# Kernel tuning notes

Measured on AMD Instinct MI355X. Metric: run time of the kernel, lower is better.

The kernel has to match this reference:

```python
import jax, jax.numpy as jnp
from jax import lax
import numpy as np

N_CLASS = 5
B, T = 2048, 2048


def setup_inputs() -> dict:
    key = jax.random.key(0)
    k1, k2 = jax.random.split(key)
    x = jax.random.normal(k1, (B, T, N_CLASS), dtype=jnp.float32)
    mask = jnp.ones((B, T), dtype=jnp.int32)
    transform = jax.random.normal(k2, (N_CLASS + 2, N_CLASS + 2), dtype=jnp.float32)
    return {"x": x, "mask": mask, "transform": transform}


def reference(x, mask, transform):
    # Batched Viterbi decode. x:[B,T,C], mask:[B,T], transform:[C+2,C+2]
    Bb, Tt, C = x.shape
    START, END = C, C + 1
    trans = transform[:C, :C]                      # [C,C] prev -> curr
    mb = mask.astype(bool)

    dp0 = x[:, 0, :] + transform[START, :C][None]  # [B,C]

    def step(dp, inp):
        xt, mt = inp                               # xt:[B,C], mt:[B]
        sc = dp[:, :, None] + trans[None]          # [B,C_prev,C_curr]
        bp = jnp.argmax(sc, axis=1)                # [B,C]
        new_dp = jnp.max(sc, axis=1) + xt          # [B,C]
        dp_out = jnp.where(mt[:, None], new_dp, dp)
        # identity backpointer on padded steps so backtrace is a no-op there
        bp_out = jnp.where(mt[:, None], bp, jnp.arange(C)[None, :])
        return dp_out, bp_out

    xs = (jnp.moveaxis(x[:, 1:, :], 1, 0),         # [T-1,B,C]
          jnp.moveaxis(mb[:, 1:], 1, 0))           # [T-1,B]
    dp, bps = lax.scan(step, dp0, xs)              # bps: [T-1,B,C]

    final = dp + transform[:C, END][None]          # [B,C]
    max_score = jnp.max(final, axis=1)             # [B]
    last = jnp.argmax(final, axis=1)               # [B]

    def back(idx, bp):
        prev = jnp.take_along_axis(bp, idx[:, None], axis=1)[:, 0]
        return prev, idx

    first, rest = lax.scan(back, last, bps, reverse=True)  # rest: [T-1,B]
    path = jnp.concatenate([first[None], rest], axis=0)    # [T,B]
    return max_score, path.T                                # [B], [B,T]
```

## Files before the change

### kernel.cpp

```cpp
#include <hip/hip_runtime.h>
#include <cstdint>

#define B_    2048
#define T_    2048
#define TD    7
#define NCHK  128
#define IDENT 0x4688u

__device__ __forceinline__ uint32_t mcompose(uint32_t f, uint32_t g) {
    uint32_t r = 0;
#pragma unroll
    for (int j = 0; j < 5; ++j) {
        uint32_t gj = (g >> (3 * j)) & 7u;
        r |= ((f >> (3 * gj)) & 7u) << (3 * j);
    }
    return r;
}

__device__ __forceinline__ uint32_t cvtpk(float lo, float hi) {
    uint32_t r;
    asm("v_cvt_pk_bf16_f32 %0, %1, %2" : "=v"(r) : "v"(lo), "v"(hi));
    return r;
}

__device__ __forceinline__ float bfld(const uint16_t* __restrict__ xs, int h) {
    return __uint_as_float(((uint32_t)xs[h]) << 16);
}

template<bool P>
__device__ __forceinline__ void hstep(const uint16_t* __restrict__ xs, int h, bool pred,
                                      float (&dp)[5], const float (&tr)[5][5]) {
    float nd[5];
#pragma unroll
    for (int j = 0; j < 5; ++j) {
        float v = fmaxf(fmaxf(fmaxf(fmaxf(dp[0] + tr[0][j], dp[1] + tr[1][j]),
                                    dp[2] + tr[2][j]), dp[3] + tr[3][j]),
                        dp[4] + tr[4][j]);
        nd[j] = v + bfld(xs, h + j);
    }
#pragma unroll
    for (int j = 0; j < 5; ++j) dp[j] = (P && !pred) ? dp[j] : nd[j];
}

template<bool SEL>
__device__ __forceinline__ uint32_t lstep(const uint16_t* __restrict__ xs, int h, bool mm,
                                          float (&dp)[5], const float (&tr)[5][5],
                                          uint32_t& rho) {
    float nd[5]; int aa[5]; uint32_t pk = 0;
#pragma unroll
    for (int j = 0; j < 5; ++j) {
        float s[5];
#pragma unroll
        for (int i = 0; i < 5; ++i) {
            float f = dp[i] + tr[i][j];
            uint32_t u = (__float_as_uint(f) & ~7u) | (uint32_t)(7 - i);
            s[i] = __uint_as_float(u);
        }
        float m = fmaxf(fmaxf(fmaxf(fmaxf(s[0], s[1]), s[2]), s[3]), s[4]);
        int a = 7 - (int)(__float_as_uint(m) & 7u);
        float v = m + bfld(xs, h + j);
        if (SEL) { a = mm ? a : j; nd[j] = mm ? v : dp[j]; }
        else     { nd[j] = v; }
        aa[j] = a;
        pk |= ((uint32_t)a) << (3 * j);
    }
    uint32_t nr = 0;
#pragma unroll
    for (int j = 0; j < 5; ++j) nr |= ((rho >> (3 * aa[j])) & 7u) << (3 * j);
    rho = nr;
#pragma unroll
    for (int j = 0; j < 5; ++j) dp[j] = nd[j];
    return pk;
}

template<bool AM>
__device__ __forceinline__ void fwd(const uint16_t* __restrict__ xs,
                                    const uint16_t* __restrict__ msk, int cc,
                                    const float (&tr)[5][5], const float (&ts)[5],
                                    float (&dp)[5], float (&dpE)[5],
                                    uint32_t (&acc)[8], uint32_t& rho) {
    const int hbase = (cc > 0) ? 82 * (cc - 1) : 0;
#pragma unroll
    for (int j = 0; j < 5; ++j) dp[j] = bfld(xs, hbase + j);
    if (cc <= 1) {
#pragma unroll
        for (int j = 0; j < 5; ++j) dp[j] += ts[j];
    }
    const uint32_t mh = AM ? 0xFFFFu : ((cc > 0) ? (uint32_t)msk[cc - 1] : 0u);
#pragma unroll
    for (int h = 1; h <= 15; ++h) {
        if (AM) hstep<false>(xs, hbase + 5 * h, true, dp, tr);
        else    hstep<true >(xs, hbase + 5 * h, ((mh >> h) & 1u) != 0, dp, tr);
    }
    if (AM && cc == 0) {
#pragma unroll
        for (int j = 0; j < 5; ++j) dp[j] = bfld(xs, j) + ts[j];
    }
#pragma unroll
    for (int j = 0; j < 5; ++j) dpE[j] = (cc == 0) ? 0.0f : dp[j];

    rho = IDENT;
    const int lb = 82 * cc;
    const uint32_t ml = AM ? 0xFFFFu : (uint32_t)msk[cc];
    acc[0] = lstep<true>(xs, lb, (cc != 0) && ((ml & 1u) != 0), dp, tr, rho);
#pragma unroll
    for (int l = 1; l < 16; ++l) {
        uint32_t pk;
        if (AM) pk = lstep<false>(xs, lb + 5 * l, true, dp, tr, rho);
        else    pk = lstep<true >(xs, lb + 5 * l, ((ml >> l) & 1u) != 0, dp, tr, rho);
        if (l & 1) acc[l >> 1] |= pk << 16;
        else       acc[l >> 1]  = pk;
    }
}

__global__ __launch_bounds__(128, 3) void k_all(
    const float* __restrict__ x, const int* __restrict__ mask,
    const float* __restrict__ tf, float* __restrict__ out)
{
    __shared__ uint16_t xs[10496];
    __shared__ uint16_t msk[NCHK];
    __shared__ uint32_t tot[2];
    __shared__ float    part[2];
    __shared__ int      lastS;

    const int b = blockIdx.x, c = threadIdx.x;
    const int lane = c & 63, w = c >> 6;

    const float4* gx = (const float4*)(x + (size_t)b * (T_ * 5));
    const int4*   gm = (const int4*)(mask + (size_t)b * T_);

    float4 va[10]; int4 m4[4];
#pragma unroll
    for (int q = 0; q < 10; ++q) va[q] = gx[c + 128 * q];
#pragma unroll
    for (int q = 0; q < 4; ++q) m4[q] = gm[4 * c + q];
    __builtin_amdgcn_sched_barrier(0);
    float4 vb[10];
#pragma unroll
    for (int q = 0; q < 10; ++q) vb[q] = gx[c + 128 * (10 + q)];
    __builtin_amdgcn_sched_barrier(0);

#pragma unroll
    for (int q = 0; q < 10; ++q) {
        int fi = c + 128 * q;
        int e0 = 4 * fi;
        int k  = (e0 * 52429) >> 22;
        int h0 = e0 + 2 * k;
        *(uint32_t*)(xs + h0)     = cvtpk(va[q].x, va[q].y);
        *(uint32_t*)(xs + h0 + 2) = cvtpk(va[q].z, va[q].w);
    }
    uint32_t mb = 0;
#pragma unroll
    for (int q = 0; q < 4; ++q) {
        mb |= (m4[q].x ? 1u : 0u) << (4 * q);
        mb |= (m4[q].y ? 1u : 0u) << (4 * q + 1);
        mb |= (m4[q].z ? 1u : 0u) << (4 * q + 2);
        mb |= (m4[q].w ? 1u : 0u) << (4 * q + 3);
    }
    msk[c] = (uint16_t)mb;
#pragma unroll
    for (int q = 0; q < 10; ++q) {
        int fi = c + 128 * (10 + q);
        int e0 = 4 * fi;
        int k  = (e0 * 52429) >> 22;
        int h0 = e0 + 2 * k;
        *(uint32_t*)(xs + h0)     = cvtpk(vb[q].x, vb[q].y);
        *(uint32_t*)(xs + h0 + 2) = cvtpk(vb[q].z, vb[q].w);
    }

    float tr[5][5], ts[5], te[5];
#pragma unroll
    for (int i = 0; i < 5; ++i)
#pragma unroll
        for (int j = 0; j < 5; ++j) tr[i][j] = tf[i * TD + j];
#pragma unroll
    for (int j = 0; j < 5; ++j) ts[j] = tf[5 * TD + j];
#pragma unroll
    for (int j = 0; j < 5; ++j) te[j] = tf[j * TD + 6];

    const int allones = __syncthreads_and(mb == 0xFFFFu);

    float dp[5], dpE[5]; uint32_t acc[8], rho;
    if (allones) fwd<true >(xs, msk, c, tr, ts, dp, dpE, acc, rho);
    else         fwd<false>(xs, msk, c, tr, ts, dp, dpE, acc, rho);

    float svec[5];
#pragma unroll
    for (int j = 0; j < 5; ++j) {
        int r = (rho >> (3 * j)) & 7;
        float e = dpE[0];
        e = (r == 1) ? dpE[1] : e;
        e = (r == 2) ? dpE[2] : e;
        e = (r == 3) ? dpE[3] : e;
        e = (r == 4) ? dpE[4] : e;
        svec[j] = dp[j] - e;
    }

    uint32_t I = rho;
#pragma unroll
    for (int d = 1; d < 64; d <<= 1) {
        uint32_t oth = __shfl_down(I, d);
        uint32_t cm  = mcompose(I, oth);
        I = (lane + d < 64) ? cm : I;
    }
    if (lane == 0) tot[w] = I;
    if (c == NCHK - 1) {
        float best = dp[0] + te[0]; int last = 0;
#pragma unroll
        for (int j = 1; j < 5; ++j) {
            float s = dp[j] + te[j];
            if (s > best) { best = s; last = j; }
        }
        lastS = last;
    }
    __syncthreads();

    uint32_t Tw = (w == 0) ? tot[1] : IDENT;
    uint32_t Ex = __shfl_down(I, 1);
    uint32_t M  = (lane < 63) ? mcompose(Ex, Tw) : Tw;
    const int last = lastS;
    const int ec = (M >> (3 * last)) & 7;

    {
        float v = svec[0];
        v = (ec == 1) ? svec[1] : v;
        v = (ec == 2) ? svec[2] : v;
        v = (ec == 3) ? svec[3] : v;
        v = (ec == 4) ? svec[4] : v;
        if (c == NCHK - 1) v += te[last];
#pragma unroll
        for (int off = 1; off < 64; off <<= 1) v += __shfl_xor(v, off);
        if (lane == 0) part[w] = v;
    }
    __syncthreads();
    if (c == 0) out[b] = part[0] + part[1];

    float pv[16];
    int e = ec;
#pragma unroll
    for (int l = 15; l >= 0; --l) {
        pv[l] = (float)e;
        uint32_t p = (acc[l >> 1] >> (16 * (l & 1))) & 0xFFFFu;
        e = (p >> (3 * e)) & 7;
    }
    float* path = out + B_ + (size_t)b * T_ + c * 16;
#pragma unroll
    for (int q = 0; q < 4; ++q) {
        float4 v; v.x = pv[4*q]; v.y = pv[4*q+1]; v.z = pv[4*q+2]; v.w = pv[4*q+3];
        ((float4*)path)[q] = v;
    }
}

extern "C" void kernel_launch(void* const* d_in, const int* in_sizes, int n_in,
                              void* d_out, int out_size, void* d_ws, size_t ws_size,
                              hipStream_t stream) {
    const float* x         = (const float*)d_in[0];
    const int*   mask      = (const int*)d_in[1];
    const float* transform = (const float*)d_in[2];
    float*       out       = (float*)d_out;

    hipLaunchKernelGGL(k_all, dim3(B_), dim3(128), 0, stream,
                       x, mask, transform, out);
}
```

Before: 38.71 us.

## Preload per-chunk bf16 inputs into registers via 16-byte LDS reads

Changes the shared-memory padding so each 80-element chunk starts on a 16-byte boundary (stride 88 halves). Each thread then loads its two chunks (halo and local) into 40-word register arrays with vectorized uint4 reads, replacing many scalar 16-bit LDS loads. Global-to-LDS stores become 8-byte writes, the sched barriers are dropped, and launch bounds drop from 3 to 2 waves per EU to make room for the extra 80 registers. The trade is fewer LDS instructions against higher register pressure and lower occupancy.

```diff
diff --git a/kernel.cpp b/kernel.cpp
--- a/kernel.cpp
+++ b/kernel.cpp
@@ -23,12 +23,14 @@
     return r;
 }
 
-__device__ __forceinline__ float bfld(const uint16_t* __restrict__ xs, int h) {
-    return __uint_as_float(((uint32_t)xs[h]) << 16);
-}
+__device__ __forceinline__ float xget(const uint32_t (&w)[40], int h) {
+    return (h & 1) ? __uint_as_float(w[h >> 1] & 0xFFFF0000u)
+                   : __uint_as_float(w[h >> 1] << 16);
+}
+
 
 template<bool P>
-__device__ __forceinline__ void hstep(const uint16_t* __restrict__ xs, int h, bool pred,
+__device__ __forceinline__ void hstep(const uint32_t (&w)[40], int base, bool pred,
                                       float (&dp)[5], const float (&tr)[5][5]) {
     float nd[5];
 #pragma unroll
@@ -36,14 +38,14 @@
         float v = fmaxf(fmaxf(fmaxf(fmaxf(dp[0] + tr[0][j], dp[1] + tr[1][j]),
                                     dp[2] + tr[2][j]), dp[3] + tr[3][j]),
                         dp[4] + tr[4][j]);
-        nd[j] = v + bfld(xs, h + j);
+        nd[j] = v + xget(w, base + j);
     }
 #pragma unroll
     for (int j = 0; j < 5; ++j) dp[j] = (P && !pred) ? dp[j] : nd[j];
 }
 
 template<bool SEL>
-__device__ __forceinline__ uint32_t lstep(const uint16_t* __restrict__ xs, int h, bool mm,
+__device__ __forceinline__ uint32_t lstep(const uint32_t (&w)[40], int base, bool mm,
                                           float (&dp)[5], const float (&tr)[5][5],
                                           uint32_t& rho) {
     float nd[5]; int aa[5]; uint32_t pk = 0;
@@ -58,7 +60,7 @@
         }
         float m = fmaxf(fmaxf(fmaxf(fmaxf(s[0], s[1]), s[2]), s[3]), s[4]);
         int a = 7 - (int)(__float_as_uint(m) & 7u);
-        float v = m + bfld(xs, h + j);
+        float v = m + xget(w, base + j);
         if (SEL) { a = mm ? a : j; nd[j] = mm ? v : dp[j]; }
         else     { nd[j] = v; }
         aa[j] = a;
@@ -79,9 +81,23 @@
                                     const float (&tr)[5][5], const float (&ts)[5],
                                     float (&dp)[5], float (&dpE)[5],
                                     uint32_t (&acc)[8], uint32_t& rho) {
-    const int hbase = (cc > 0) ? 82 * (cc - 1) : 0;
-#pragma unroll
-    for (int j = 0; j < 5; ++j) dp[j] = bfld(xs, hbase + j);
+    const int hc = (cc > 0) ? cc - 1 : 0;
+    const uint4* hp = (const uint4*)(xs + 88 * hc);
+    const uint4* lp = (const uint4*)(xs + 88 * cc);
+    uint32_t hw[40], lw[40];
+#pragma unroll
+    for (int q = 0; q < 10; ++q) {
+        uint4 t = hp[q];
+        hw[4*q] = t.x; hw[4*q+1] = t.y; hw[4*q+2] = t.z; hw[4*q+3] = t.w;
+    }
+#pragma unroll
+    for (int q = 0; q < 10; ++q) {
+        uint4 t = lp[q];
+        lw[4*q] = t.x; lw[4*q+1] = t.y; lw[4*q+2] = t.z; lw[4*q+3] = t.w;
+    }
+
+#pragma unroll
+    for (int j = 0; j < 5; ++j) dp[j] = xget(hw, j);
     if (cc <= 1) {
 #pragma unroll
         for (int j = 0; j < 5; ++j) dp[j] += ts[j];
@@ -89,35 +105,34 @@
     const uint32_t mh = AM ? 0xFFFFu : ((cc > 0) ? (uint32_t)msk[cc - 1] : 0u);
 #pragma unroll
     for (int h = 1; h <= 15; ++h) {
-        if (AM) hstep<false>(xs, hbase + 5 * h, true, dp, tr);
-        else    hstep<true >(xs, hbase + 5 * h, ((mh >> h) & 1u) != 0, dp, tr);
+        if (AM) hstep<false>(hw, 5 * h, true, dp, tr);
+        else    hstep<true >(hw, 5 * h, ((mh >> h) & 1u) != 0, dp, tr);
     }
     if (AM && cc == 0) {
 #pragma unroll
-        for (int j = 0; j < 5; ++j) dp[j] = bfld(xs, j) + ts[j];
+        for (int j = 0; j < 5; ++j) dp[j] = xget(hw, j) + ts[j];
     }
 #pragma unroll
     for (int j = 0; j < 5; ++j) dpE[j] = (cc == 0) ? 0.0f : dp[j];
 
     rho = IDENT;
-    const int lb = 82 * cc;
     const uint32_t ml = AM ? 0xFFFFu : (uint32_t)msk[cc];
-    acc[0] = lstep<true>(xs, lb, (cc != 0) && ((ml & 1u) != 0), dp, tr, rho);
+    acc[0] = lstep<true>(lw, 0, (cc != 0) && ((ml & 1u) != 0), dp, tr, rho);
 #pragma unroll
     for (int l = 1; l < 16; ++l) {
         uint32_t pk;
-        if (AM) pk = lstep<false>(xs, lb + 5 * l, true, dp, tr, rho);
-        else    pk = lstep<true >(xs, lb + 5 * l, ((ml >> l) & 1u) != 0, dp, tr, rho);
+        if (AM) pk = lstep<false>(lw, 5 * l, true, dp, tr, rho);
+        else    pk = lstep<true >(lw, 5 * l, ((ml >> l) & 1u) != 0, dp, tr, rho);
         if (l & 1) acc[l >> 1] |= pk << 16;
         else       acc[l >> 1]  = pk;
     }
 }
 
-__global__ __launch_bounds__(128, 3) void k_all(
+__global__ __launch_bounds__(128, 2) void k_all(
     const float* __restrict__ x, const int* __restrict__ mask,
     const float* __restrict__ tf, float* __restrict__ out)
 {
-    __shared__ uint16_t xs[10496];
+    __shared__ __align__(16) uint16_t xs[11264];
     __shared__ uint16_t msk[NCHK];
     __shared__ uint32_t tot[2];
     __shared__ float    part[2];
@@ -129,25 +144,22 @@
     const float4* gx = (const float4*)(x + (size_t)b * (T_ * 5));
     const int4*   gm = (const int4*)(mask + (size_t)b * T_);
 
-    float4 va[10]; int4 m4[4];
+    float4 va[10], vb[10]; int4 m4[4];
 #pragma unroll
     for (int q = 0; q < 10; ++q) va[q] = gx[c + 128 * q];
 #pragma unroll
     for (int q = 0; q < 4; ++q) m4[q] = gm[4 * c + q];
-    __builtin_amdgcn_sched_barrier(0);
-    float4 vb[10];
 #pragma unroll
     for (int q = 0; q < 10; ++q) vb[q] = gx[c + 128 * (10 + q)];
-    __builtin_amdgcn_sched_barrier(0);
 
 #pragma unroll
     for (int q = 0; q < 10; ++q) {
         int fi = c + 128 * q;
         int e0 = 4 * fi;
         int k  = (e0 * 52429) >> 22;
-        int h0 = e0 + 2 * k;
-        *(uint32_t*)(xs + h0)     = cvtpk(va[q].x, va[q].y);
-        *(uint32_t*)(xs + h0 + 2) = cvtpk(va[q].z, va[q].w);
+        int h0 = e0 + 8 * k;
+        uint2 p; p.x = cvtpk(va[q].x, va[q].y); p.y = cvtpk(va[q].z, va[q].w);
+        *(uint2*)(xs + h0) = p;
     }
     uint32_t mb = 0;
 #pragma unroll
@@ -163,9 +175,9 @@
         int fi = c + 128 * (10 + q);
         int e0 = 4 * fi;
         int k  = (e0 * 52429) >> 22;
-        int h0 = e0 + 2 * k;
-        *(uint32_t*)(xs + h0)     = cvtpk(vb[q].x, vb[q].y);
-        *(uint32_t*)(xs + h0 + 2) = cvtpk(vb[q].z, vb[q].w);
+        int h0 = e0 + 8 * k;
+        uint2 p; p.x = cvtpk(vb[q].x, vb[q].y); p.y = cvtpk(vb[q].z, vb[q].w);
+        *(uint2*)(xs + h0) = p;
     }
 
     float tr[5][5], ts[5], te[5];
```

Result: slower. 41.66 us (+7.6%).
